# Performance work log

Measured on AMD Instinct MI355X. Metric: run time of the kernel, lower is better.

## Reference

```python
import jax, jax.numpy as jnp
import numpy as np

V, D, H, L, B, S = 32000, 512, 512, 2, 64, 64
PAD = 0
NEG = -1000000000.0


def setup_inputs() -> dict:
    key = jax.random.key(0)
    ks = jax.random.split(key, 12)
    s = 0.05
    X = jax.random.randint(ks[0], (B, S), 0, V)
    enc = jax.random.normal(ks[1], (B, S - 1, H), jnp.float32)
    mask = jnp.zeros((S - 1, S - 1), dtype=bool)
    emb = jax.random.normal(ks[2], (V, D), jnp.float32) * s
    lstm_Wih = jax.random.normal(ks[3], (L, 4 * H, D), jnp.float32) * s  # D == H so stacking works for layer>0
    lstm_Whh = jax.random.normal(ks[4], (L, 4 * H, H), jnp.float32) * s
    lstm_bih = jax.random.normal(ks[5], (L, 4 * H), jnp.float32) * s
    lstm_bhh = jax.random.normal(ks[6], (L, 4 * H), jnp.float32) * s
    attn_Wh = jax.random.normal(ks[7], (H, H), jnp.float32) * s  # attn weight cols acting on decoder hidden
    attn_We = jax.random.normal(ks[8], (H, H), jnp.float32) * s  # attn weight cols acting on encoder outputs
    attn_b = jax.random.normal(ks[9], (H,), jnp.float32) * s
    v_w = jax.random.normal(ks[10], (H,), jnp.float32) * s
    fc_W = jax.random.normal(ks[11], (V, 2 * H), jnp.float32) * s
    fc_b = jnp.zeros((V,), jnp.float32)
    return {"X": X, "encoderOutputs": enc, "mask": mask, "emb": emb,
            "lstm_Wih": lstm_Wih, "lstm_Whh": lstm_Whh, "lstm_bih": lstm_bih, "lstm_bhh": lstm_bhh,
            "attn_Wh": attn_Wh, "attn_We": attn_We, "attn_b": attn_b, "v_w": v_w,
            "fc_W": fc_W, "fc_b": fc_b}


def _forward(X, enc, mask, emb, Wih, Whh, bih, bhh, attn_Wh, attn_We, attn_b, v_w, fc_W, fc_b):
    Bn, Sn = X.shape
    T = Sn - 1
    E = emb[X[:, :-1]]  # [B,T,D]
    # encoder part of attention projection is time-invariant: hoist out of the loop
    enc_proj = jnp.einsum('beh,kh->bek', enc, attn_We) + attn_b  # [B,T,H]
    h0 = jnp.zeros((L, Bn, H), E.dtype)
    c0 = jnp.zeros((L, Bn, H), E.dtype)
    xs = (jnp.transpose(E, (1, 0, 2)), X[:, 1:].T, jnp.arange(T))

    def step(carry, x_t):
        h, c = carry
        e_t, tgt, t = x_t
        inp = e_t
        hs, cs = [], []
        for l in range(L):  # fixed small layer loop
            g = inp @ Wih[l].T + h[l] @ Whh[l].T + bih[l] + bhh[l]
            i, f, gg, o = jnp.split(g, 4, axis=-1)  # torch gate order i,f,g,o
            cn = jax.nn.sigmoid(f) * c[l] + jax.nn.sigmoid(i) * jnp.tanh(gg)
            hn = jax.nn.sigmoid(o) * jnp.tanh(cn)
            hs.append(hn); cs.append(cn)
            inp = hn
        h = jnp.stack(hs); c = jnp.stack(cs)
        top = inp  # [B,H] == LSTM output of last layer
        energy = jnp.tanh((top @ attn_Wh.T)[:, None, :] + enc_proj)  # [B,T,H]
        scores = energy @ v_w  # [B,T]
        # original: self.mask[t-1] (python negative wrap) then mask.unsqueeze(0).unsqueeze(1)
        m = mask[(t - 1) % mask.shape[0], :T]  # [T]
        s3 = jnp.where(m[None, None, :], NEG, scores[None])  # broadcast -> [1,B,T]
        att = jax.nn.softmax(s3, axis=1)[0]  # softmax over batch dim, as in original
        weighted = jnp.einsum('be,beh->bh', att, enc)
        logits = jnp.concatenate([top, weighted], axis=1) @ fc_W.T + fc_b  # [B,V]
        logp = jax.nn.log_softmax(logits, axis=-1)
        nll = -jnp.take_along_axis(logp, tgt[:, None], axis=1)[:, 0]
        valid = tgt != PAD
        loss_t = jnp.sum(jnp.where(valid, nll, 0.0)) / jnp.sum(valid)  # CE mean with ignore_index
        return (h, c), loss_t

    _, losses = jax.lax.scan(step, (h0, c0), xs)
    return jnp.mean(losses)  # totalLoss / (seq_len - 1)


def reference(X, encoderOutputs, mask, emb, lstm_Wih, lstm_Whh, lstm_bih, lstm_bhh, attn_Wh, attn_We, attn_b, v_w, fc_W, fc_b):
    return _forward(X, encoderOutputs, mask, emb, lstm_Wih, lstm_Whh, lstm_bih, lstm_bhh, attn_Wh, attn_We, attn_b, v_w, fc_W, fc_b)
```

## Files before the change

kernel.cpp:

```cpp
#include <hip/hip_runtime.h>
#include <math.h>

#define NEGV -1000000000.0f

typedef unsigned short u16;
typedef __attribute__((ext_vector_type(8))) short bf16x8;
typedef __attribute__((ext_vector_type(4))) float f32x4;

__device__ __forceinline__ u16 f2bf(float f){
  union { float f; unsigned u; } v; v.f = f;
  unsigned u = v.u;
  unsigned r = (u + 0x7fffu + ((u >> 16) & 1u)) >> 16;
  return (u16)r;
}
__device__ __forceinline__ float bf2f(u16 b){
  union { unsigned u; float f; } v; v.u = ((unsigned)b) << 16;
  return v.f;
}
__device__ __forceinline__ float sigmf(float x){ return 1.f / (1.f + __expf(-x)); }
__device__ __forceinline__ float tanhf_(float x){
  float e = __expf(-2.f * fabsf(x));
  float t = (1.f - e) / (1.f + e);
  return x >= 0.f ? t : -t;
}
__device__ __forceinline__ float wred64(float v){
  #pragma unroll
  for (int m = 32; m; m >>= 1) v += __shfl_xor(v, m, 64);
  return v;
}
__device__ __forceinline__ float wmax64(float v){
  #pragma unroll
  for (int m = 32; m; m >>= 1) v = fmaxf(v, __shfl_xor(v, m, 64));
  return v;
}

typedef const __attribute__((address_space(1))) unsigned int* gas_ptr;
typedef __attribute__((address_space(3))) unsigned int* las_ptr;
__device__ __forceinline__ void gl_lds16(const u16* g, u16* l){
  __builtin_amdgcn_global_load_lds((gas_ptr)g, (las_ptr)l, 16, 0, 0);
}

__device__ __forceinline__ void st_sc1_u16(u16* p, unsigned v){
  asm volatile("global_store_short %0, %1, off sc1" :: "v"(p), "v"(v) : "memory");
}

__device__ __forceinline__ void cvt4(u16* d, const float* s){
  float4 v = *(const float4*)s;
  union { u16 h[4]; uint2 u; } o;
  o.h[0] = f2bf(v.x); o.h[1] = f2bf(v.y); o.h[2] = f2bf(v.z); o.h[3] = f2bf(v.w);
  *(uint2*)d = o.u;
}
__global__ __launch_bounds__(256) void k_prep(
    const float* wih, const float* whh, const float* we, const float* wh,
    const float* fcw, const float* enc, const float* bih, const float* bhh,
    u16* wihb, u16* whhb, u16* web, u16* whb, u16* fcwb, u16* encb, float* b01)
{
  const long n0 = 2097152, n1 = 2097152, n2 = 262144, n3 = 262144;
  const long n4 = 32768000, n5 = 2064384, n6 = 4096;
  const long total4 = (n0 + n1 + n2 + n3 + n4 + n5 + n6) >> 2;
  long stride = (long)gridDim.x * 256;
  for (long i = (long)blockIdx.x * 256 + threadIdx.x; i < total4; i += stride){
    long j = i << 2;
    if (j < n0){ cvt4(wihb + j, wih + j); continue; } j -= n0;
    if (j < n1){ cvt4(whhb + j, whh + j); continue; } j -= n1;
    if (j < n2){ cvt4(web + j,  we + j);  continue; } j -= n2;
    if (j < n3){ cvt4(whb + j,  wh + j);  continue; } j -= n3;
    if (j < n4){ cvt4(fcwb + j, fcw + j); continue; } j -= n4;
    if (j < n5){ cvt4(encb + j, enc + j); continue; } j -= n5;
    float4 a = *(const float4*)(bih + j);
    float4 b = *(const float4*)(bhh + j);
    *(float4*)(b01 + j) = make_float4(a.x + b.x, a.y + b.y, a.z + b.z, a.w + b.w);
  }
}

__global__ __launch_bounds__(256) void k_embed(const int* X, const float* emb, u16* ebf){
  int row = blockIdx.x;
  int t = row >> 6, b = row & 63;
  int tok = X[b * 64 + t];
  const float* src = emb + (long)tok * 512;
  u16* dst = ebf + (long)row * 512;
  for (int j = threadIdx.x; j < 512; j += 256) dst[j] = f2bf(src[j]);
}

__global__ __launch_bounds__(256) void gemm_bt(
    const u16* Am, int lda, const u16* Bm, int ldb,
    float* C, int ldc, const float* bias, int K)
{
  __shared__ u16 sA[64 * 32], sB[64 * 32];
  int tm = blockIdx.x, tn = blockIdx.y;
  int tid = threadIdx.x;
  int wave = tid >> 6, lane = tid & 63;
  int wm = wave >> 1, wn = wave & 1;
  int q = lane >> 4, cl = lane & 15;
  f32x4 acc[2][2];
  #pragma unroll
  for (int i = 0; i < 2; i++)
    #pragma unroll
    for (int j = 0; j < 2; j++) acc[i][j] = (f32x4){0.f, 0.f, 0.f, 0.f};

  int r = tid >> 2, ck = tid & 3;
  const u16* Ags = Am + (long)(tm * 64 + r) * lda + ck * 8;
  const u16* Bgs = Bm + (long)(tn * 64 + r) * ldb + ck * 8;
  u16* sAw = &sA[wave * 512];
  u16* sBw = &sB[wave * 512];

  for (int kt = 0; kt < K; kt += 32){
    gl_lds16(Ags + kt, sAw);
    gl_lds16(Bgs + kt, sBw);
    __syncthreads();
    #pragma unroll
    for (int i = 0; i < 2; i++){
      bf16x8 af = *(const bf16x8*)&sA[(wm * 32 + i * 16 + cl) * 32 + q * 8];
      #pragma unroll
      for (int j = 0; j < 2; j++){
        bf16x8 bfv = *(const bf16x8*)&sB[(wn * 32 + j * 16 + cl) * 32 + q * 8];
        acc[i][j] = __builtin_amdgcn_mfma_f32_16x16x32_bf16(af, bfv, acc[i][j], 0, 0, 0);
      }
    }
    __syncthreads();
  }
  #pragma unroll
  for (int i = 0; i < 2; i++)
    #pragma unroll
    for (int j = 0; j < 2; j++){
      int colg = tn * 64 + wn * 32 + j * 16 + cl;
      float bv = bias ? bias[colg] : 0.f;
      #pragma unroll
      for (int rr = 0; rr < 4; rr++){
        int rowg = tm * 64 + wm * 32 + i * 16 + q * 4 + rr;
        C[(long)rowg * ldc + colg] = acc[i][j][rr] + bv;
      }
    }
}

__global__ __launch_bounds__(256) void gemm_btb(
    const u16* Am, int lda, const u16* Bm, int ldb,
    u16* C, int ldc, const float* bias, int K)
{
  __shared__ u16 sA[64 * 32], sB[64 * 32];
  int tm = blockIdx.x, tn = blockIdx.y;
  int tid = threadIdx.x;
  int wave = tid >> 6, lane = tid & 63;
  int wm = wave >> 1, wn = wave & 1;
  int q = lane >> 4, cl = lane & 15;
  f32x4 acc[2][2];
  #pragma unroll
  for (int i = 0; i < 2; i++)
    #pragma unroll
    for (int j = 0; j < 2; j++) acc[i][j] = (f32x4){0.f, 0.f, 0.f, 0.f};

  int r = tid >> 2, ck = tid & 3;
  const u16* Ags = Am + (long)(tm * 64 + r) * lda + ck * 8;
  const u16* Bgs = Bm + (long)(tn * 64 + r) * ldb + ck * 8;
  u16* sAw = &sA[wave * 512];
  u16* sBw = &sB[wave * 512];

  for (int kt = 0; kt < K; kt += 32){
    gl_lds16(Ags + kt, sAw);
    gl_lds16(Bgs + kt, sBw);
    __syncthreads();
    #pragma unroll
    for (int i = 0; i < 2; i++){
      bf16x8 af = *(const bf16x8*)&sA[(wm * 32 + i * 16 + cl) * 32 + q * 8];
      #pragma unroll
      for (int j = 0; j < 2; j++){
        bf16x8 bfv = *(const bf16x8*)&sB[(wn * 32 + j * 16 + cl) * 32 + q * 8];
        acc[i][j] = __builtin_amdgcn_mfma_f32_16x16x32_bf16(af, bfv, acc[i][j], 0, 0, 0);
      }
    }
    __syncthreads();
  }
  #pragma unroll
  for (int i = 0; i < 2; i++)
    #pragma unroll
    for (int j = 0; j < 2; j++){
      int colg = tn * 64 + wn * 32 + j * 16 + cl;
      float bv = bias ? bias[colg] : 0.f;
      #pragma unroll
      for (int rr = 0; rr < 4; rr++){
        int rowg = tm * 64 + wm * 32 + i * 16 + q * 4 + rr;
        C[(long)rowg * ldc + colg] = f2bf(acc[i][j][rr] + bv);
      }
    }
}

__device__ __forceinline__ void wait_flags(int* flags, int tid, int need0, int need1){
  if (tid < 64){
    int need = (tid < 32) ? need0 : need1;
    for (;;){
      int v = __hip_atomic_load(flags + tid, __ATOMIC_RELAXED, __HIP_MEMORY_SCOPE_AGENT);
      if (__ballot(v >= need) == ~0ull) break;
    }
  }
  __syncthreads();
}

#define ISSUE_RING_FRAGS(afr, Ab)                                              \
  {                                                                            \
    _Pragma("unroll")                                                          \
    for (int kt = 0; kt < 16; kt++)                                            \
      asm volatile("global_load_dwordx4 %0, %1, off offset:%2 sc1"             \
                   : "=v"(afr[kt]) : "v"(Ab), "i"(kt * 64));                   \
  }
#define WAITCNT_VM(N)                                                          \
  { asm volatile("s_waitcnt vmcnt(" #N ")" ::: "memory");                      \
    __builtin_amdgcn_sched_barrier(0); }

__global__ __launch_bounds__(256, 1) void lstm_pipe(
    const u16* whh0, const u16* wih1, const u16* whh1,
    const u16* x0b, const float* b1s,
    u16* ring0, u16* ring1, u16* feat, int* flags)
{
  __shared__ u16 sW[32768];
  __shared__ u16 sW2[32768];
  int wg = blockIdx.x;
  int layer = wg >> 5;
  int cc = (wg & 31) * 16;
  int tid = threadIdx.x;
  int wave = tid >> 6, lane = tid & 63;
  int q = lane >> 4, cl = lane & 15;
  int j = cc + cl;

  {
    const u16* src = layer ? whh1 : whh0;
    for (int ch = tid; ch < 4096; ch += 256){
      int row = ch >> 6, c = ch & 63;
      int g = row >> 4, r = row & 15;
      *(uint4*)&sW[((c * 4 + g) * 16 + r) * 8] =
          *(const uint4*)&src[(long)(g * 512 + cc + r) * 512 + c * 8];
      if (layer)
        *(uint4*)&sW2[((c * 4 + g) * 16 + r) * 8] =
            *(const uint4*)&wih1[(long)(g * 512 + cc + r) * 512 + c * 8];
    }
  }
  __syncthreads();

  float cst[4] = {0.f, 0.f, 0.f, 0.f};
  float bg[4];
  if (layer){
    #pragma unroll
    for (int g = 0; g < 4; g++) bg[g] = b1s[g * 512 + j];
  }

  int foff = (wave * 16 + cl) * 512 + q * 8;

  for (int t = 0; t < 63; t++){
    f32x4 acc[4];
    #pragma unroll
    for (int g = 0; g < 4; g++) acc[g] = (f32x4){0.f, 0.f, 0.f, 0.f};

    if (layer == 0){
      float xg[4][4];
      #pragma unroll
      for (int rr = 0; rr < 4; rr++){
        int s = wave * 16 + q * 4 + rr;
        const u16* xr = x0b + (long)(t * 64 + s) * 2048 + j;
        #pragma unroll
        for (int g = 0; g < 4; g++) xg[g][rr] = bf2f(xr[g * 512]);
      }
      wait_flags(flags, tid, t, t - 7);
      {
        const u16* Ab = ring0 + ((t + 7) & 7) * 32768 + foff;
        bf16x8 afr[16];
        ISSUE_RING_FRAGS(afr, Ab);
        WAITCNT_VM(0);
        #pragma unroll
        for (int kt = 0; kt < 16; kt++)
          #pragma unroll
          for (int g = 0; g < 4; g++){
            bf16x8 bfv = *(const bf16x8*)&sW[(((kt * 4 + q) * 4 + g) * 16 + cl) * 8];
            acc[g] = __builtin_amdgcn_mfma_f32_16x16x32_bf16(afr[kt], bfv, acc[g], 0, 0, 0);
          }
      }
      u16* hn = ring0 + (t & 7) * 32768;
      #pragma unroll
      for (int rr = 0; rr < 4; rr++){
        int s = wave * 16 + q * 4 + rr;
        float gi = acc[0][rr] + xg[0][rr];
        float gf = acc[1][rr] + xg[1][rr];
        float gg = acc[2][rr] + xg[2][rr];
        float go = acc[3][rr] + xg[3][rr];
        float cn = sigmf(gf) * cst[rr] + sigmf(gi) * tanhf_(gg);
        cst[rr] = cn;
        st_sc1_u16(hn + s * 512 + j, (unsigned)f2bf(sigmf(go) * tanhf_(cn)));
      }
    } else {
      wait_flags(flags, tid, t + 1, t);
      const u16* Ab1 = ring1 + ((t + 7) & 7) * 32768 + foff;
      const u16* Ab0 = ring0 + (t & 7) * 32768 + foff;
      bf16x8 a1[16], a0[16];
      ISSUE_RING_FRAGS(a1, Ab1);
      ISSUE_RING_FRAGS(a0, Ab0);
      WAITCNT_VM(16);
      #pragma unroll
      for (int kt = 0; kt < 16; kt++)
        #pragma unroll
        for (int g = 0; g < 4; g++){
          bf16x8 bfv = *(const bf16x8*)&sW[(((kt * 4 + q) * 4 + g) * 16 + cl) * 8];
          acc[g] = __builtin_amdgcn_mfma_f32_16x16x32_bf16(a1[kt], bfv, acc[g], 0, 0, 0);
        }
      WAITCNT_VM(0);
      #pragma unroll
      for (int kt = 0; kt < 16; kt++)
        #pragma unroll
        for (int g = 0; g < 4; g++){
          bf16x8 bfv = *(const bf16x8*)&sW2[(((kt * 4 + q) * 4 + g) * 16 + cl) * 8];
          acc[g] = __builtin_amdgcn_mfma_f32_16x16x32_bf16(a0[kt], bfv, acc[g], 0, 0, 0);
        }
      u16* hn = ring1 + (t & 7) * 32768;
      #pragma unroll
      for (int rr = 0; rr < 4; rr++){
        int s = wave * 16 + q * 4 + rr;
        float gi = acc[0][rr] + bg[0];
        float gf = acc[1][rr] + bg[1];
        float gg = acc[2][rr] + bg[2];
        float go = acc[3][rr] + bg[3];
        float cn = sigmf(gf) * cst[rr] + sigmf(gi) * tanhf_(gg);
        cst[rr] = cn;
        u16 hb = f2bf(sigmf(go) * tanhf_(cn));
        st_sc1_u16(hn + s * 512 + j, (unsigned)hb);
        feat[(long)(t * 64 + s) * 1024 + j] = hb;
      }
    }
    asm volatile("s_waitcnt vmcnt(0)" ::: "memory");
    __syncthreads();
    if (tid == 0)
      __hip_atomic_store(flags + wg, t + 1, __ATOMIC_RELAXED, __HIP_MEMORY_SCOPE_AGENT);
  }
}

__global__ __launch_bounds__(256) void k_scores(
    const float* qb, const float* encp, const float* vw, float* scores)
{
  int row = blockIdx.x;
  int b = row & 63;
  int wave = threadIdx.x >> 6, lane = threadIdx.x & 63;
  float qv[8], vwv[8];
  const float* qr = qb + (long)row * 512 + lane * 8;
  #pragma unroll
  for (int i = 0; i < 8; i++){ qv[i] = qr[i]; vwv[i] = vw[lane * 8 + i]; }
  for (int e = wave; e < 63; e += 4){
    const float* er = encp + (long)(b * 63 + e) * 512 + lane * 8;
    float s = 0.f;
    #pragma unroll
    for (int i = 0; i < 8; i++) s += vwv[i] * tanhf_(qv[i] + er[i]);
    s = wred64(s);
    if (lane == 0) scores[(long)row * 63 + e] = s;
  }
}

__global__ __launch_bounds__(64) void k_att(float* scores, const unsigned char* mask){
  int idx = blockIdx.x;
  int t = idx / 63, e = idx - t * 63;
  int lane = threadIdx.x;
  long off = (long)(t * 64 + lane) * 63 + e;
  float s = scores[off];
  if (mask[((t + 62) % 63) * 63 + e]) s = NEGV;
  float M = wmax64(s);
  float p = __expf(s - M);
  float S = wred64(p);
  scores[off] = p / S;
}

__global__ __launch_bounds__(256) void k_weighted(
    const float* att, const float* enc, u16* feat)
{
  int row = blockIdx.x;
  int b = row & 63;
  int j = threadIdx.x;
  float a0 = 0.f, a1 = 0.f;
  const float* ar = att + (long)row * 63;
  const float* er = enc + (long)b * 63 * 512;
  for (int e = 0; e < 63; e++){
    float a = ar[e];
    a0 += a * er[(long)e * 512 + j];
    a1 += a * er[(long)e * 512 + j + 256];
  }
  feat[(long)row * 1024 + 512 + j] = f2bf(a0);
  feat[(long)row * 1024 + 768 + j] = f2bf(a1);
}

__global__ __launch_bounds__(512, 1) void gemm_fc(
    const u16* Am, const u16* Bm, const float* fcb, float* partials)
{
  __shared__ u16 sA[2][16384], sB[2][16384];
  __shared__ float sm[256][4], ss[256][4];
  int tm = blockIdx.x, tn = blockIdx.y;
  int tid = threadIdx.x;
  int wave = tid >> 6, lane = tid & 63;
  int wm = wave >> 2, wn = wave & 3;
  int q = lane >> 4, cl = lane & 15;

  f32x4 acc[8][4];
  #pragma unroll
  for (int i = 0; i < 8; i++)
    #pragma unroll
    for (int j = 0; j < 4; j++) acc[i][j] = (f32x4){0.f, 0.f, 0.f, 0.f};

  const u16 *pA[4], *pB[4];
  int sdst[4];
  #pragma unroll
  for (int h = 0; h < 4; h++){
    int c = tid + h * 512;
    int row = c >> 3;
    int kc = (c & 7) ^ (row & 7);
    pA[h] = Am + (long)(tm * 256 + row) * 1024 + kc * 8;
    pB[h] = Bm + (long)(tn * 256 + row) * 1024 + kc * 8;
    sdst[h] = (h * 512 + wave * 64) * 8;
  }
  int r0 = cl * 64;
  int ex = (cl & 7) * 16;
  int e0 = ((q * 16) ^ ex) >> 1;
  int e1 = ((64 + q * 16) ^ ex) >> 1;

  #pragma unroll
  for (int h = 0; h < 4; h++){
    gl_lds16(pA[h], &sA[0][sdst[h]]);
    gl_lds16(pB[h], &sB[0][sdst[h]]);
  }
  asm volatile("s_waitcnt vmcnt(0)" ::: "memory");
  __syncthreads();

  for (int k = 0; k < 16; k++){
    int cur = k & 1;
    if (k < 15){
      int adv = (k + 1) * 64;
      #pragma unroll
      for (int h = 0; h < 4; h++){
        gl_lds16(pA[h] + adv, &sA[cur ^ 1][sdst[h]]);
        gl_lds16(pB[h] + adv, &sB[cur ^ 1][sdst[h]]);
      }
    }
    #pragma unroll
    for (int ks = 0; ks < 2; ks++){
      int eo = ks ? e1 : e0;
      bf16x8 af[8], bf[4];
      #pragma unroll
      for (int mt = 0; mt < 8; mt++)
        af[mt] = *(const bf16x8*)&sA[cur][(wm * 8 + mt) * 1024 + r0 + eo];
      #pragma unroll
      for (int nt = 0; nt < 4; nt++)
        bf[nt] = *(const bf16x8*)&sB[cur][(wn * 4 + nt) * 1024 + r0 + eo];
      __builtin_amdgcn_s_setprio(1);
      #pragma unroll
      for (int nt = 0; nt < 4; nt++)
        #pragma unroll
        for (int mt = 0; mt < 8; mt++)
          acc[mt][nt] = __builtin_amdgcn_mfma_f32_16x16x32_bf16(af[mt], bf[nt], acc[mt][nt], 0, 0, 0);
      __builtin_amdgcn_s_setprio(0);
    }
    asm volatile("s_waitcnt vmcnt(0)" ::: "memory");
    __syncthreads();
  }

  float fb[4];
  #pragma unroll
  for (int nt = 0; nt < 4; nt++) fb[nt] = fcb[tn * 256 + wn * 64 + nt * 16 + cl];
  #pragma unroll
  for (int mt = 0; mt < 8; mt++){
    #pragma unroll
    for (int rr = 0; rr < 4; rr++){
      float vals[4];
      float vm = -3.0e38f, vs = 0.f;
      #pragma unroll
      for (int nt = 0; nt < 4; nt++){ float v = acc[mt][nt][rr] + fb[nt]; vals[nt] = v; vm = fmaxf(vm, v); }
      #pragma unroll
      for (int nt = 0; nt < 4; nt++) vs += __expf(vals[nt] - vm);
      #pragma unroll
      for (int m = 1; m < 16; m <<= 1){
        float om = __shfl_xor(vm, m, 16);
        float os = __shfl_xor(vs, m, 16);
        float nm = fmaxf(vm, om);
        vs = vs * __expf(vm - nm) + os * __expf(om - nm);
        vm = nm;
      }
      if (cl == 0){
        int rl = wm * 128 + mt * 16 + q * 4 + rr;
        sm[rl][wn] = vm; ss[rl][wn] = vs;
      }
    }
  }
  __syncthreads();
  if (tid < 256){
    float M = -3.0e38f;
    #pragma unroll
    for (int w = 0; w < 4; w++) M = fmaxf(M, sm[tid][w]);
    float S = 0.f;
    #pragma unroll
    for (int w = 0; w < 4; w++) S += ss[tid][w] * __expf(sm[tid][w] - M);
    long row = tm * 256 + tid;
    partials[(row * 125 + tn) * 2]     = M;
    partials[(row * 125 + tn) * 2 + 1] = S;
  }
}

__global__ __launch_bounds__(256) void k_rowstats(
    const float* partials, const u16* feat, const u16* fcwb,
    const float* fcb, const int* X, float* nll)
{
  int row = blockIdx.x * 4 + (threadIdx.x >> 6);
  int lane = threadIdx.x & 63;
  if (row >= 4032) return;
  float vm = -3.0e38f, vs = 0.f;
  const float* pr = partials + (long)row * 250;
  for (int i = lane; i < 125; i += 64){
    float m = pr[i * 2], s2 = pr[i * 2 + 1];
    float nm = fmaxf(vm, m);
    vs = vs * __expf(vm - nm) + s2 * __expf(m - nm);
    vm = nm;
  }
  #pragma unroll
  for (int m = 32; m; m >>= 1){
    float om = __shfl_xor(vm, m, 64);
    float os = __shfl_xor(vs, m, 64);
    float nm = fmaxf(vm, om);
    vs = vs * __expf(vm - nm) + os * __expf(om - nm);
    vm = nm;
  }
  float logZ = vm + __logf(vs);
  int t = row >> 6, b = row & 63;
  int tgt = X[b * 64 + t + 1];
  const u16* fr = feat + (long)row * 1024 + lane * 16;
  const u16* wr = fcwb + (long)tgt * 1024 + lane * 16;
  float d = 0.f;
  #pragma unroll
  for (int i = 0; i < 16; i++) d += bf2f(fr[i]) * bf2f(wr[i]);
  d = wred64(d);
  if (lane == 0) nll[row] = logZ - (d + fcb[tgt]);
}

__global__ __launch_bounds__(256) void k_final(const float* nll, const int* X, float* out){
  __shared__ float lt[64];
  int wave = threadIdx.x >> 6, lane = threadIdx.x & 63;
  for (int t = wave; t < 63; t += 4){
    int tgt = X[lane * 64 + t + 1];
    float v = (tgt != 0) ? nll[t * 64 + lane] : 0.f;
    float c = (tgt != 0) ? 1.f : 0.f;
    v = wred64(v); c = wred64(c);
    if (lane == 0) lt[t] = v / c;
  }
  __syncthreads();
  if (threadIdx.x == 0){
    float s = 0.f;
    for (int t = 0; t < 63; t++) s += lt[t];
    out[0] = s / 63.f;
  }
}

extern "C" void kernel_launch(void* const* d_in, const int* in_sizes, int n_in,
                              void* d_out, int out_size, void* d_ws, size_t ws_size,
                              hipStream_t stream)
{
  (void)in_sizes; (void)n_in; (void)out_size; (void)ws_size;
  const int*   X    = (const int*)d_in[0];
  const float* enc  = (const float*)d_in[1];
  const unsigned char* mask = (const unsigned char*)d_in[2];
  const float* emb  = (const float*)d_in[3];
  const float* wih  = (const float*)d_in[4];
  const float* whh  = (const float*)d_in[5];
  const float* bih  = (const float*)d_in[6];
  const float* bhh  = (const float*)d_in[7];
  const float* awh  = (const float*)d_in[8];
  const float* awe  = (const float*)d_in[9];
  const float* ab   = (const float*)d_in[10];
  const float* vw   = (const float*)d_in[11];
  const float* fcw  = (const float*)d_in[12];
  const float* fcb  = (const float*)d_in[13];
  float* out = (float*)d_out;

  char* w = (char*)d_ws;
  size_t o = 0;
  auto alloc = [&](size_t bytes){ size_t r = o; o = (o + bytes + 255) & ~(size_t)255; return r; };
  size_t o_ebf  = alloc((size_t)4032 * 512 * 2);
  size_t o_wihb = alloc((size_t)2 * 2048 * 512 * 2);
  size_t o_whhb = alloc((size_t)2 * 2048 * 512 * 2);
  size_t o_web  = alloc((size_t)512 * 512 * 2);
  size_t o_whb  = alloc((size_t)512 * 512 * 2);
  size_t o_fcwb = alloc((size_t)32000 * 1024 * 2);
  size_t o_encb = alloc((size_t)4032 * 512 * 2);
  size_t o_b01  = alloc((size_t)4096 * 4);
  size_t o_x0   = alloc((size_t)4032 * 2048 * 2);
  size_t o_encp = alloc((size_t)4032 * 512 * 4);
  size_t o_q    = alloc((size_t)4032 * 512 * 4);
  size_t o_feat = alloc((size_t)4096 * 1024 * 2);
  size_t o_ring = alloc((size_t)2 * 8 * 32768 * 2);
  size_t o_flags= alloc((size_t)512);
  size_t o_sc   = alloc((size_t)63 * 64 * 63 * 4);
  size_t o_part = alloc((size_t)4096 * 250 * 2 * 4);
  size_t o_nll  = alloc((size_t)4032 * 4);

  u16* ebf   = (u16*)(w + o_ebf);
  u16* wihb  = (u16*)(w + o_wihb);
  u16* whhb  = (u16*)(w + o_whhb);
  u16* web   = (u16*)(w + o_web);
  u16* whb   = (u16*)(w + o_whb);
  u16* fcwb  = (u16*)(w + o_fcwb);
  u16* encb  = (u16*)(w + o_encb);
  float* b01 = (float*)(w + o_b01);
  u16* x0b   = (u16*)(w + o_x0);
  float* encp= (float*)(w + o_encp);
  float* qb  = (float*)(w + o_q);
  u16* feat  = (u16*)(w + o_feat);
  u16* ring0 = (u16*)(w + o_ring);
  u16* ring1 = ring0 + 8 * 32768;
  int* flags = (int*)(w + o_flags);
  float* sc  = (float*)(w + o_sc);
  float* part= (float*)(w + o_part);
  float* nllb= (float*)(w + o_nll);

  hipMemsetAsync(w + o_ring, 0, (o_flags - o_ring) + 512, stream);

  k_prep<<<4096, 256, 0, stream>>>(wih, whh, awe, awh, fcw, enc, bih, bhh,
                                   wihb, whhb, web, whb, fcwb, encb, b01);
  k_embed<<<4032, 256, 0, stream>>>(X, emb, ebf);

  gemm_btb<<<dim3(63, 32), 256, 0, stream>>>(ebf, 512, wihb, 512, x0b, 2048, b01, 512);
  gemm_bt<<<dim3(63, 8), 256, 0, stream>>>(encb, 512, web, 512, encp, 512, ab, 512);

  lstm_pipe<<<64, 256, 0, stream>>>(whhb, wihb + 2048 * 512, whhb + 2048 * 512,
                                    x0b, b01 + 2048, ring0, ring1, feat, flags);

  gemm_bt<<<dim3(63, 8), 256, 0, stream>>>(feat, 1024, whb, 512, qb, 512, nullptr, 512);
  k_scores<<<4032, 256, 0, stream>>>(qb, encp, vw, sc);
  k_att<<<3969, 64, 0, stream>>>(sc, mask);
  k_weighted<<<4032, 256, 0, stream>>>(sc, enc, feat);

  gemm_fc<<<dim3(16, 125), 512, 0, stream>>>(feat, fcwb, fcb, part);
  k_rowstats<<<1008, 256, 0, stream>>>(part, feat, fcwb, fcb, X, nllb);
  k_final<<<1, 256, 0, stream>>>(nllb, X, out);
}
```

Before: 1.270 ms.

## Split FC GEMM k-tiles into half-stages with finer waitcnt and swizzled block order

```diff
diff --git a/kernel.cpp b/kernel.cpp
--- a/kernel.cpp
+++ b/kernel.cpp
@@ -383,9 +383,11 @@
 __global__ __launch_bounds__(512, 1) void gemm_fc(
     const u16* Am, const u16* Bm, const float* fcb, float* partials)
 {
-  __shared__ u16 sA[2][16384], sB[2][16384];
+  __shared__ u16 sA[2][2][8192], sB[2][2][8192];
   __shared__ float sm[256][4], ss[256][4];
-  int tm = blockIdx.x, tn = blockIdx.y;
+  int lin = blockIdx.y * 16 + blockIdx.x;
+  int nl  = (lin & 7) * 250 + (lin >> 3);
+  int tm = nl & 15, tn = nl >> 4;
   int tid = threadIdx.x;
   int wave = tid >> 6, lane = tid & 63;
   int wm = wave >> 2, wn = wave & 3;
@@ -397,60 +399,59 @@
     #pragma unroll
     for (int j = 0; j < 4; j++) acc[i][j] = (f32x4){0.f, 0.f, 0.f, 0.f};
 
-  const u16 *pA[4], *pB[4];
-  int sdst[4];
-  #pragma unroll
-  for (int h = 0; h < 4; h++){
-    int c = tid + h * 512;
-    int row = c >> 3;
-    int kc = (c & 7) ^ (row & 7);
-    pA[h] = Am + (long)(tm * 256 + row) * 1024 + kc * 8;
-    pB[h] = Bm + (long)(tn * 256 + row) * 1024 + kc * 8;
-    sdst[h] = (h * 512 + wave * 64) * 8;
-  }
-  int r0 = cl * 64;
-  int ex = (cl & 7) * 16;
-  int e0 = ((q * 16) ^ ex) >> 1;
-  int e1 = ((64 + q * 16) ^ ex) >> 1;
-
-  #pragma unroll
-  for (int h = 0; h < 4; h++){
-    gl_lds16(pA[h], &sA[0][sdst[h]]);
-    gl_lds16(pB[h], &sB[0][sdst[h]]);
-  }
-  asm volatile("s_waitcnt vmcnt(0)" ::: "memory");
-  __syncthreads();
+  const u16 *bA[2][2], *bB[2][2];
+  #pragma unroll
+  for (int ks = 0; ks < 2; ks++)
+    #pragma unroll
+    for (int i = 0; i < 2; i++){
+      int r = i * 128 + (tid >> 2);
+      int kc4 = (tid & 3) ^ (r & 3);
+      bA[ks][i] = Am + (long)(tm * 256 + r) * 1024 + ks * 32 + kc4 * 8;
+      bB[ks][i] = Bm + (long)(tn * 256 + r) * 1024 + ks * 32 + kc4 * 8;
+    }
+  int sd0 = (wave * 64) * 8;
+  int sd1 = (512 + wave * 64) * 8;
+
+  #define STAGE_GROUP(adv, ks, buf)                            \
+    { gl_lds16(bA[ks][0] + (adv), &sA[buf][ks][sd0]);          \
+      gl_lds16(bA[ks][1] + (adv), &sA[buf][ks][sd1]);          \
+      gl_lds16(bB[ks][0] + (adv), &sB[buf][ks][sd0]);          \
+      gl_lds16(bB[ks][1] + (adv), &sB[buf][ks][sd1]); }
+
+  int qx8 = (q ^ (cl & 3)) * 8;
+
+  #define COMPUTE_HALF(buf, ks)                                                     \
+    { bf16x8 af[8], bfv[4];                                                         \
+      _Pragma("unroll")                                                             \
+      for (int mt = 0; mt < 8; mt++)                                                \
+        af[mt] = *(const bf16x8*)&sA[buf][ks][(wm * 128 + mt * 16 + cl) * 32 + qx8];\
+      _Pragma("unroll")                                                             \
+      for (int nt = 0; nt < 4; nt++)                                                \
+        bfv[nt] = *(const bf16x8*)&sB[buf][ks][(wn * 64 + nt * 16 + cl) * 32 + qx8];\
+      __builtin_amdgcn_s_setprio(1);                                                \
+      _Pragma("unroll")                                                             \
+      for (int nt = 0; nt < 4; nt++)                                                \
+        _Pragma("unroll")                                                           \
+        for (int mt = 0; mt < 8; mt++)                                              \
+          acc[mt][nt] = __builtin_amdgcn_mfma_f32_16x16x32_bf16(af[mt], bfv[nt],    \
+                                                                acc[mt][nt], 0, 0, 0);\
+      __builtin_amdgcn_s_setprio(0); }
+
+  STAGE_GROUP(0, 0, 0);
+  STAGE_GROUP(0, 1, 0);
 
   for (int k = 0; k < 16; k++){
     int cur = k & 1;
-    if (k < 15){
-      int adv = (k + 1) * 64;
-      #pragma unroll
-      for (int h = 0; h < 4; h++){
-        gl_lds16(pA[h] + adv, &sA[cur ^ 1][sdst[h]]);
-        gl_lds16(pB[h] + adv, &sB[cur ^ 1][sdst[h]]);
-      }
-    }
-    #pragma unroll
-    for (int ks = 0; ks < 2; ks++){
-      int eo = ks ? e1 : e0;
-      bf16x8 af[8], bf[4];
-      #pragma unroll
-      for (int mt = 0; mt < 8; mt++)
-        af[mt] = *(const bf16x8*)&sA[cur][(wm * 8 + mt) * 1024 + r0 + eo];
-      #pragma unroll
-      for (int nt = 0; nt < 4; nt++)
-        bf[nt] = *(const bf16x8*)&sB[cur][(wn * 4 + nt) * 1024 + r0 + eo];
-      __builtin_amdgcn_s_setprio(1);
-      #pragma unroll
-      for (int nt = 0; nt < 4; nt++)
-        #pragma unroll
-        for (int mt = 0; mt < 8; mt++)
-          acc[mt][nt] = __builtin_amdgcn_mfma_f32_16x16x32_bf16(af[mt], bf[nt], acc[mt][nt], 0, 0, 0);
-      __builtin_amdgcn_s_setprio(0);
-    }
-    asm volatile("s_waitcnt vmcnt(0)" ::: "memory");
+    int adv = (k + 1) * 64;
+    WAITCNT_VM(4);
     __syncthreads();
+    if (k < 15) STAGE_GROUP(adv, 0, cur ^ 1);
+    COMPUTE_HALF(cur, 0);
+    if (k < 15) { WAITCNT_VM(4); }
+    else        { WAITCNT_VM(0); }
+    __syncthreads();
+    if (k < 15) STAGE_GROUP(adv, 1, cur ^ 1);
+    COMPUTE_HALF(cur, 1);
   }
 
   float fb[4];
@@ -492,6 +493,8 @@
     partials[(row * 125 + tn) * 2]     = M;
     partials[(row * 125 + tn) * 2 + 1] = S;
   }
+  #undef STAGE_GROUP
+  #undef COMPUTE_HALF
 }
 
 __global__ __launch_bounds__(256) void k_rowstats(
```

Result: slower. 1.327 ms (+4.5%).
